# Kernel optimization log

Hardware: AMD Instinct MI355X
Metric: run time of the kernel (lower is better)

The kernel has to match this reference:

```python
import jax, jax.numpy as jnp
import numpy as np

DIM = 1024
HEADS = 16
HEAD_DIM = DIM // HEADS
D_FF = 4 * DIM
EPS = 1e-5


def layer_norm(x, gamma, beta):
    mu = jnp.mean(x, axis=-1, keepdims=True)
    var = jnp.var(x, axis=-1, keepdims=True)
    return (x - mu) * jax.lax.rsqrt(var + EPS) * gamma + beta


def linear_attention(x, w_qkv, b_qkv, w_out, b_out):
    B, S, D = x.shape
    qkv = x @ w_qkv + b_qkv  # [B,S,3D]
    qkv = qkv.reshape(B, S, 3, HEADS, HEAD_DIM)
    q, k, v = qkv[:, :, 0], qkv[:, :, 1], qkv[:, :, 2]  # [B,S,H,Dh]
    q = jax.nn.softmax(q, axis=-1)       # feature-dim softmax
    k = jax.nn.softmax(k, axis=1)        # sequence-dim softmax
    kv = jnp.einsum('bshd,bshe->bhde', k, v)   # [B,H,Dh,Dh]
    out = jnp.einsum('bshd,bhde->bshe', q, kv)  # [B,S,H,Dh]
    out = out.reshape(B, S, D)
    return out @ w_out + b_out


def setup_inputs() -> dict:
    key = jax.random.key(0)
    ks = jax.random.split(key, 10)
    s = lambda fan_in: 1.0 / np.sqrt(fan_in)
    return {
        'x': jax.random.normal(ks[0], (4, 4096, DIM), dtype=jnp.float32),
        'w_qkv': jax.random.normal(ks[1], (DIM, 3 * DIM), jnp.float32) * s(DIM),
        'b_qkv': jnp.zeros((3 * DIM,), jnp.float32),
        'w_attn_out': jax.random.normal(ks[2], (DIM, DIM), jnp.float32) * s(DIM),
        'b_attn_out': jnp.zeros((DIM,), jnp.float32),
        'w_ffn1': jax.random.normal(ks[3], (DIM, D_FF), jnp.float32) * s(DIM),
        'b_ffn1': jnp.zeros((D_FF,), jnp.float32),
        'w_ffn2': jax.random.normal(ks[4], (D_FF, DIM), jnp.float32) * s(D_FF),
        'b_ffn2': jnp.zeros((DIM,), jnp.float32),
        'g1': jnp.ones((DIM,), jnp.float32),
        'beta1': jnp.zeros((DIM,), jnp.float32),
        'g2': jnp.ones((DIM,), jnp.float32),
        'beta2': jnp.zeros((DIM,), jnp.float32),
    }


def reference(x, w_qkv, b_qkv, w_attn_out, b_attn_out, w_ffn1, b_ffn1,
              w_ffn2, b_ffn2, g1, beta1, g2, beta2):
    # h = attn(norm1(x)); out = x + ffn(norm2(x + h))  (dropout=0)
    h = linear_attention(layer_norm(x, g1, beta1), w_qkv, b_qkv, w_attn_out, b_attn_out)
    z = layer_norm(x + h, g2, beta2)
    delta = jax.nn.gelu(z @ w_ffn1 + b_ffn1, approximate=False) @ w_ffn2 + b_ffn2
    return x + delta
```

## Files before the change

kernel.cpp:

```cpp
#include <hip/hip_runtime.h>
#include <hip/hip_bf16.h>
#include <cstdint>
#include <cstddef>

#define DIMC 1024
#define HEADS 16
#define HD 64
#define DFF 4096
#define BB 4
#define SS 4096
#define NROWS (BB*SS)

typedef __bf16 bf16_t;
typedef __bf16 bf16x8 __attribute__((ext_vector_type(8)));
typedef __bf16 bf16x4 __attribute__((ext_vector_type(4)));
typedef float  f32x4  __attribute__((ext_vector_type(4)));

#define GLDS16(gp, lp) \
  __builtin_amdgcn_global_load_lds((const __attribute__((address_space(1))) void*)(gp), \
                                   (__attribute__((address_space(3))) void*)(lp), 16, 0, 0)

#define MFMA16(a, b, c) __builtin_amdgcn_mfma_f32_16x16x32_bf16((a), (b), (c), 0, 0, 0)

__device__ __forceinline__ float fast_erf(float x) {
  float ax = fabsf(x);
  float t  = __builtin_amdgcn_rcpf(fmaf(0.3275911f, ax, 1.0f));
  float p  = t * fmaf(t, fmaf(t, fmaf(t, fmaf(t, 1.061405429f, -1.453152027f),
                                      1.421413741f), -0.284496736f), 0.254829592f);
  float er = 1.0f - p * __expf(-ax * ax);
  return copysignf(er, x);
}

__global__ __launch_bounds__(256) void prep_kernel(const float* __restrict__ w_qkv,
                                                   const float* __restrict__ w_out,
                                                   const float* __restrict__ w_ffn1,
                                                   const float* __restrict__ w_ffn2,
                                                   bf16_t* __restrict__ WT_QKV,
                                                   bf16_t* __restrict__ WT_OUT,
                                                   bf16_t* __restrict__ WT_FFN1,
                                                   bf16_t* __restrict__ WT_FFN2,
                                                   const float* __restrict__ x,
                                                   const float* __restrict__ gamma,
                                                   const float* __restrict__ beta,
                                                   bf16_t* __restrict__ act1) {
  const int bid = blockIdx.x;
  if (bid < 12288) {
    const float* W; bf16_t* Wt; int K, N, bx, by;
    if (bid < 3072)      { W = w_qkv;  Wt = WT_QKV;  K = 1024; N = 3072; bx = bid % 96;           by = bid / 96; }
    else if (bid < 4096) { W = w_out;  Wt = WT_OUT;  K = 1024; N = 1024; bx = (bid - 3072) % 32;  by = (bid - 3072) / 32; }
    else if (bid < 8192) { W = w_ffn1; Wt = WT_FFN1; K = 1024; N = 4096; bx = (bid - 4096) % 128; by = (bid - 4096) / 128; }
    else                 { W = w_ffn2; Wt = WT_FFN2; K = 4096; N = 1024; bx = (bid - 8192) % 32;  by = (bid - 8192) / 32; }
    __shared__ float tile[32][33];
    const int tx = threadIdx.x & 31, ty = threadIdx.x >> 5;
    const int c0 = bx * 32, r0 = by * 32;
    #pragma unroll
    for (int i = 0; i < 32; i += 8)
      tile[ty + i][tx] = W[(long)(r0 + ty + i) * N + c0 + tx];
    __syncthreads();
    #pragma unroll
    for (int i = 0; i < 32; i += 8)
      Wt[(long)(c0 + ty + i) * K + r0 + tx] = (bf16_t)tile[tx][ty + i];
  } else {
    long r = bid - 12288;
    int t = threadIdx.x;
    float4 v = ((const float4*)(x + r * DIMC))[t];
    float s  = v.x + v.y + v.z + v.w;
    float sq = v.x * v.x + v.y * v.y + v.z * v.z + v.w * v.w;
    #pragma unroll
    for (int o = 32; o > 0; o >>= 1) { s += __shfl_xor(s, o); sq += __shfl_xor(sq, o); }
    __shared__ float red[8];
    if ((t & 63) == 0) { red[(t >> 6) * 2] = s; red[(t >> 6) * 2 + 1] = sq; }
    __syncthreads();
    s  = red[0] + red[2] + red[4] + red[6];
    sq = red[1] + red[3] + red[5] + red[7];
    float mu  = s * (1.0f / DIMC);
    float var = sq * (1.0f / DIMC) - mu * mu;
    float rs  = 1.0f / sqrtf(var + 1e-5f);
    float4 g  = ((const float4*)gamma)[t];
    float4 bb = ((const float4*)beta)[t];
    bf16x4 o;
    o[0] = (bf16_t)((v.x - mu) * rs * g.x + bb.x);
    o[1] = (bf16_t)((v.y - mu) * rs * g.y + bb.y);
    o[2] = (bf16_t)((v.z - mu) * rs * g.z + bb.z);
    o[3] = (bf16_t)((v.w - mu) * rs * g.w + bb.w);
    ((bf16x4*)(act1 + r * DIMC))[t] = o;
  }
}

__global__ __launch_bounds__(256) void ln_bf16(const bf16_t* __restrict__ in,
                                               const float* __restrict__ gamma,
                                               const float* __restrict__ beta,
                                               bf16_t* __restrict__ out) {
  long r = blockIdx.x;
  int t = threadIdx.x;
  bf16x4 v4 = ((const bf16x4*)(in + r * DIMC))[t];
  float v0 = v4[0], v1 = v4[1], v2 = v4[2], v3 = v4[3];
  float s  = v0 + v1 + v2 + v3;
  float sq = v0 * v0 + v1 * v1 + v2 * v2 + v3 * v3;
  #pragma unroll
  for (int o = 32; o > 0; o >>= 1) { s += __shfl_xor(s, o); sq += __shfl_xor(sq, o); }
  __shared__ float red[8];
  if ((t & 63) == 0) { red[(t >> 6) * 2] = s; red[(t >> 6) * 2 + 1] = sq; }
  __syncthreads();
  s  = red[0] + red[2] + red[4] + red[6];
  sq = red[1] + red[3] + red[5] + red[7];
  float mu  = s * (1.0f / DIMC);
  float var = sq * (1.0f / DIMC) - mu * mu;
  float rs  = 1.0f / sqrtf(var + 1e-5f);
  float4 g  = ((const float4*)gamma)[t];
  float4 bb = ((const float4*)beta)[t];
  bf16x4 o;
  o[0] = (bf16_t)((v0 - mu) * rs * g.x + bb.x);
  o[1] = (bf16_t)((v1 - mu) * rs * g.y + bb.y);
  o[2] = (bf16_t)((v2 - mu) * rs * g.z + bb.z);
  o[3] = (bf16_t)((v3 - mu) * rs * g.w + bb.w);
  ((bf16x4*)(out + r * DIMC))[t] = o;
}

template <int MODE>
__global__ __launch_bounds__(256, 2) void gemm_bt(const bf16_t* __restrict__ A,
                                                  const bf16_t* __restrict__ Bt,
                                                  const float* __restrict__ bias,
                                                  const float* __restrict__ resid,
                                                  void* __restrict__ outp,
                                                  int M, int N, int K, int lda, long bstride) {
  __shared__ bf16_t As[128 * 64];
  __shared__ bf16_t Bs[128 * 64];
  const int t = threadIdx.x;
  const int lane = t & 63;
  const int wave = t >> 6;

  const int nwg  = gridDim.x * gridDim.y;
  const int bid0 = blockIdx.y * gridDim.x + blockIdx.x;
  const int lg   = (bid0 & 7) * (nwg >> 3) + (bid0 >> 3);
  const int span = (int)gridDim.y << 2;
  const int gidx = lg / span;
  const int rem  = lg - gidx * span;
  const long arow0 = (long)(rem >> 2) * 128;
  const long brow0 = (long)((gidx << 2) + (rem & 3)) * 128;

  const bf16_t* BtB = Bt + (arow0 >> 12) * bstride;

  const int wm = (wave >> 1) * 64, wn = (wave & 1) * 64;

  f32x4 acc[4][4] = {};
  const int fr  = lane & 15;
  const int q4  = lane >> 4;
  const int frl = fr & 7;
  const int cr0 = ((q4    ) ^ frl) * 8;
  const int cr1 = ((q4 + 4) ^ frl) * 8;

  for (int kt = 0; kt < K; kt += 64) {
    #pragma unroll
    for (int p = 0; p < 4; ++p) {
      const int c = t + 256 * p;
      const int row = c >> 3;
      const int gch = ((c & 7) ^ (row & 7)) * 8;
      GLDS16(A   + (arow0 + row) * (long)lda + kt + gch, &As[c * 8]);
      GLDS16(BtB + (brow0 + row) * (long)K   + kt + gch, &Bs[c * 8]);
    }
    asm volatile("s_waitcnt vmcnt(0)" ::: "memory");
    __syncthreads();
    {
      bf16x8 a[4], b[4];
      #pragma unroll
      for (int i = 0; i < 4; ++i) {
        a[i] = *(const bf16x8*)&As[(wm + i * 16 + fr) * 64 + cr0];
        b[i] = *(const bf16x8*)&Bs[(wn + i * 16 + fr) * 64 + cr0];
      }
      #pragma unroll
      for (int i = 0; i < 4; ++i)
        #pragma unroll
        for (int j = 0; j < 4; ++j)
          acc[i][j] = MFMA16(a[i], b[j], acc[i][j]);
      #pragma unroll
      for (int i = 0; i < 4; ++i) {
        a[i] = *(const bf16x8*)&As[(wm + i * 16 + fr) * 64 + cr1];
        b[i] = *(const bf16x8*)&Bs[(wn + i * 16 + fr) * 64 + cr1];
      }
      #pragma unroll
      for (int i = 0; i < 4; ++i)
        #pragma unroll
        for (int j = 0; j < 4; ++j)
          acc[i][j] = MFMA16(a[i], b[j], acc[i][j]);
    }
    __syncthreads();
  }

  const int rq = q4 * 4;

  if (MODE == 3 && brow0 < 1024) {
    float bv[4];
    #pragma unroll
    for (int j = 0; j < 4; ++j) bv[j] = bias[brow0 + wn + j * 16 + fr];
    #pragma unroll
    for (int i = 0; i < 4; ++i) {
      #pragma unroll
      for (int r = 0; r < 4; ++r) {
        float v[4];
        #pragma unroll
        for (int j = 0; j < 4; ++j) v[j] = acc[i][j][r] + bv[j];
        float m = fmaxf(fmaxf(v[0], v[1]), fmaxf(v[2], v[3]));
        #pragma unroll
        for (int o = 1; o <= 8; o <<= 1) m = fmaxf(m, __shfl_xor(m, o));
        float e[4], s = 0.f;
        #pragma unroll
        for (int j = 0; j < 4; ++j) { e[j] = __expf(v[j] - m); s += e[j]; }
        #pragma unroll
        for (int o = 1; o <= 8; o <<= 1) s += __shfl_xor(s, o);
        float inv = 1.0f / s;
        long row = arow0 + wm + i * 16 + rq + r;
        #pragma unroll
        for (int j = 0; j < 4; ++j)
          ((bf16_t*)outp)[row * N + brow0 + wn + j * 16 + fr] = (bf16_t)(e[j] * inv);
      }
    }
  } else {
    #pragma unroll
    for (int i = 0; i < 4; ++i) {
      #pragma unroll
      for (int j = 0; j < 4; ++j) {
        long col = brow0 + wn + j * 16 + fr;
        float bv = bias[col];
        #pragma unroll
        for (int r = 0; r < 4; ++r) {
          long row = arow0 + wm + i * 16 + rq + r;
          float v = acc[i][j][r] + bv;
          if (MODE == 0 || MODE == 3) {
            ((bf16_t*)outp)[row * N + col] = (bf16_t)v;
          } else if (MODE == 1) {
            ((float*)outp)[row * N + col] = v + resid[row * N + col];
          } else if (MODE == 4) {
            ((bf16_t*)outp)[row * N + col] = (bf16_t)(v + resid[row * N + col]);
          } else {
            float g = 0.5f * v * (1.0f + fast_erf(v * 0.70710678118654752f));
            ((bf16_t*)outp)[row * N + col] = (bf16_t)g;
          }
        }
      }
    }
  }
}

__global__ __launch_bounds__(256) void kv_partial(const bf16_t* __restrict__ qkv,
                                                  float* __restrict__ kvp,
                                                  float* __restrict__ esump) {
  int bh = blockIdx.x, ch = blockIdx.y;
  int b = bh >> 4, h = bh & 15;
  int t = threadIdx.x;
  __shared__ float Kexp[64][65];
  __shared__ float Vs[64][66];
  int rowl = t >> 2, c0 = (t & 3) * 16;
  int dd = t >> 2, e0 = (t & 3) * 16;
  int lsq = (t & 3) * 16;
  float acc[16] = {};
  float esum = 0.f;
  for (int sb = 0; sb < 8; ++sb) {
    long s = (long)ch * 512 + sb * 64 + rowl;
    const bf16_t* base = qkv + ((long)b * SS + s) * 3072 + h * 64;
    bf16x8 k0 = *(const bf16x8*)(base + 1024 + c0);
    bf16x8 k1 = *(const bf16x8*)(base + 1024 + c0 + 8);
    bf16x8 v0 = *(const bf16x8*)(base + 2048 + c0);
    bf16x8 v1 = *(const bf16x8*)(base + 2048 + c0 + 8);
    __syncthreads();
    #pragma unroll
    for (int j = 0; j < 8; ++j) {
      Kexp[rowl][c0 + j]     = __expf((float)k0[j]);
      Kexp[rowl][c0 + 8 + j] = __expf((float)k1[j]);
      Vs[rowl][c0 + j]       = (float)v0[j];
      Vs[rowl][c0 + 8 + j]   = (float)v1[j];
    }
    __syncthreads();
    for (int ls = 0; ls < 64; ++ls) {
      float kd = Kexp[ls][dd];
      f32x4 va0 = *(const f32x4*)&Vs[ls][e0];
      f32x4 va1 = *(const f32x4*)&Vs[ls][e0 + 4];
      f32x4 va2 = *(const f32x4*)&Vs[ls][e0 + 8];
      f32x4 va3 = *(const f32x4*)&Vs[ls][e0 + 12];
      #pragma unroll
      for (int j = 0; j < 4; ++j) {
        acc[j]      += kd * va0[j];
        acc[j + 4]  += kd * va1[j];
        acc[j + 8]  += kd * va2[j];
        acc[j + 12] += kd * va3[j];
      }
    }
    #pragma unroll
    for (int l2 = 0; l2 < 16; ++l2) esum += Kexp[lsq + l2][dd];
  }
  float* dst = kvp + (long)(bh * 8 + ch) * 4096 + dd * 64 + e0;
  #pragma unroll
  for (int j = 0; j < 16; ++j) dst[j] = acc[j];
  esum += __shfl_xor(esum, 1);
  esum += __shfl_xor(esum, 2);
  if ((t & 3) == 0) esump[(long)(bh * 8 + ch) * 64 + dd] = esum;
}

__global__ void kv_reduce(const float* __restrict__ kvp, const float* __restrict__ esump,
                          bf16_t* __restrict__ kvN) {
  int bh = blockIdx.x, t = threadIdx.x;
  __shared__ float ei[64];
  if (t < 64) {
    float es = 0.f;
    #pragma unroll
    for (int c = 0; c < 8; ++c) es += esump[(long)(bh * 8 + c) * 64 + t];
    ei[t] = 1.0f / es;
  }
  __syncthreads();
  for (int p = t; p < 4096; p += 256) {
    int d = p >> 6;
    float s = 0.f;
    #pragma unroll
    for (int c = 0; c < 8; ++c) s += kvp[(long)(bh * 8 + c) * 4096 + p];
    kvN[(long)bh * 4096 + p] = (bf16_t)(s * ei[d]);
  }
}

__global__ __launch_bounds__(256) void kv_wout(const bf16_t* __restrict__ kvN,
                                               const bf16_t* __restrict__ WT_OUT,
                                               bf16_t* __restrict__ MBT) {
  const int jt = blockIdx.x;
  const int bh = blockIdx.y;
  const int b  = bh >> 4, h = bh & 15;
  const int t = threadIdx.x, lane = t & 63, wave = t >> 6;
  __shared__ bf16_t Ws[256 * 64];
  __shared__ bf16_t Ks[64 * 64];
  const int fr = lane & 15, q4 = lane >> 4, frl = fr & 7;
  const int cr0 = ((q4    ) ^ frl) * 8;
  const int cr1 = ((q4 + 4) ^ frl) * 8;
  #pragma unroll
  for (int p = 0; p < 8; ++p) {
    const int c = t + 256 * p;
    const int row = c >> 3;
    const int gch = ((c & 7) ^ (row & 7)) * 8;
    GLDS16(WT_OUT + (long)(jt * 256 + row) * 1024 + h * 64 + gch, &Ws[c * 8]);
  }
  #pragma unroll
  for (int p = 0; p < 2; ++p) {
    const int c = t + 256 * p;
    const int row = c >> 3;
    const int gch = ((c & 7) ^ (row & 7)) * 8;
    GLDS16(kvN + (long)bh * 4096 + row * 64 + gch, &Ks[c * 8]);
  }
  asm volatile("s_waitcnt vmcnt(0)" ::: "memory");
  __syncthreads();
  f32x4 acc[4][4] = {};
  const int wj = wave * 64;
  {
    bf16x8 a[4], bfr[4];
    #pragma unroll
    for (int i = 0; i < 4; ++i) {
      a[i]   = *(const bf16x8*)&Ws[(wj + i * 16 + fr) * 64 + cr0];
      bfr[i] = *(const bf16x8*)&Ks[(i * 16 + fr) * 64 + cr0];
    }
    #pragma unroll
    for (int i = 0; i < 4; ++i)
      #pragma unroll
      for (int j = 0; j < 4; ++j)
        acc[i][j] = MFMA16(a[i], bfr[j], acc[i][j]);
    #pragma unroll
    for (int i = 0; i < 4; ++i) {
      a[i]   = *(const bf16x8*)&Ws[(wj + i * 16 + fr) * 64 + cr1];
      bfr[i] = *(const bf16x8*)&Ks[(i * 16 + fr) * 64 + cr1];
    }
    #pragma unroll
    for (int i = 0; i < 4; ++i)
      #pragma unroll
      for (int j = 0; j < 4; ++j)
        acc[i][j] = MFMA16(a[i], bfr[j], acc[i][j]);
  }
  const int rq = q4 * 4;
  #pragma unroll
  for (int i = 0; i < 4; ++i)
    #pragma unroll
    for (int j = 0; j < 4; ++j)
      #pragma unroll
      for (int r = 0; r < 4; ++r)
        MBT[((long)b * 1024 + jt * 256 + wj + i * 16 + rq + r) * 1024 + h * 64 + j * 16 + fr]
            = (bf16_t)acc[i][j][r];
}

extern "C" void kernel_launch(void* const* d_in, const int* in_sizes, int n_in,
                              void* d_out, int out_size, void* d_ws, size_t ws_size,
                              hipStream_t stream) {
  (void)in_sizes; (void)n_in; (void)out_size;
  const float* x      = (const float*)d_in[0];
  const float* w_qkv  = (const float*)d_in[1];
  const float* b_qkv  = (const float*)d_in[2];
  const float* w_out  = (const float*)d_in[3];
  const float* b_out  = (const float*)d_in[4];
  const float* w_ffn1 = (const float*)d_in[5];
  const float* b_ffn1 = (const float*)d_in[6];
  const float* w_ffn2 = (const float*)d_in[7];
  const float* b_ffn2 = (const float*)d_in[8];
  const float* g1     = (const float*)d_in[9];
  const float* be1    = (const float*)d_in[10];
  const float* g2     = (const float*)d_in[11];
  const float* be2    = (const float*)d_in[12];

  char* ws = (char*)d_ws;
  constexpr size_t WT_QKV_OFF  = 0;
  constexpr size_t WT_OUT_OFF  = WT_QKV_OFF  + 6291456;
  constexpr size_t WT_FFN1_OFF = WT_OUT_OFF  + 2097152;
  constexpr size_t WT_FFN2_OFF = WT_FFN1_OFF + 8388608;
  constexpr size_t ESUMP_OFF   = WT_FFN2_OFF + 8388608;
  constexpr size_t KVP_OFF     = ESUMP_OFF   + 294912;
  constexpr size_t KVN_OFF     = KVP_OFF     + 8388608;
  constexpr size_t MBT_OFF     = KVN_OFF     + 524288;
  constexpr size_t ACT1_OFF    = MBT_OFF     + 8388608;
  constexpr size_t BIG_OFF     = ACT1_OFF    + 33554432;

  bf16_t* WT_QKV  = (bf16_t*)(ws + WT_QKV_OFF);
  bf16_t* WT_OUT  = (bf16_t*)(ws + WT_OUT_OFF);
  bf16_t* WT_FFN1 = (bf16_t*)(ws + WT_FFN1_OFF);
  bf16_t* WT_FFN2 = (bf16_t*)(ws + WT_FFN2_OFF);
  float*  ESUMP   = (float*) (ws + ESUMP_OFF);
  float*  KVP     = (float*) (ws + KVP_OFF);
  bf16_t* KVN     = (bf16_t*)(ws + KVN_OFF);
  bf16_t* MBT     = (bf16_t*)(ws + MBT_OFF);
  bf16_t* ACT1    = (bf16_t*)(ws + ACT1_OFF);
  bf16_t* QKV     = (bf16_t*)(ws + BIG_OFF);
  bf16_t* GACT    = (bf16_t*)(ws + BIG_OFF);
  bf16_t* YB      = (bf16_t*)d_out;

  const bool big_ws = ws_size >= (size_t)(BIG_OFF + 134217728ull);

  prep_kernel<<<12288 + NROWS, 256, 0, stream>>>(w_qkv, w_out, w_ffn1, w_ffn2,
                                                 WT_QKV, WT_OUT, WT_FFN1, WT_FFN2,
                                                 x, g1, be1, ACT1);

  gemm_bt<3><<<dim3(3072 / 128, NROWS / 128), 256, 0, stream>>>(ACT1, WT_QKV, b_qkv, nullptr, QKV,
                                                                NROWS, 3072, 1024, 1024, 0);

  kv_partial<<<dim3(64, 8), 256, 0, stream>>>(QKV, KVP, ESUMP);
  kv_reduce<<<64, 256, 0, stream>>>(KVP, ESUMP, KVN);
  kv_wout<<<dim3(4, 64), 256, 0, stream>>>(KVN, WT_OUT, MBT);

  gemm_bt<4><<<dim3(1024 / 128, NROWS / 128), 256, 0, stream>>>(QKV, MBT, b_out, x, YB,
                                                                NROWS, 1024, 1024, 3072, 1048576);

  ln_bf16<<<NROWS, 256, 0, stream>>>(YB, g2, be2, ACT1);

  if (big_ws) {
    gemm_bt<2><<<dim3(4096 / 128, NROWS / 128), 256, 0, stream>>>(ACT1, WT_FFN1, b_ffn1, nullptr, GACT,
                                                                  NROWS, 4096, 1024, 1024, 0);
    gemm_bt<1><<<dim3(1024 / 128, NROWS / 128), 256, 0, stream>>>(GACT, WT_FFN2, b_ffn2, x, (float*)d_out,
                                                                  NROWS, 1024, 4096, 4096, 0);
  } else {
    for (int c = 0; c < 2; ++c) {
      const long r0 = (long)c * 8192;
      gemm_bt<2><<<dim3(4096 / 128, 8192 / 128), 256, 0, stream>>>(
          ACT1 + r0 * 1024, WT_FFN1, b_ffn1, nullptr, GACT, 8192, 4096, 1024, 1024, 0);
      gemm_bt<1><<<dim3(1024 / 128, 8192 / 128), 256, 0, stream>>>(
          GACT, WT_FFN2, b_ffn2, x + r0 * 1024, (float*)d_out + r0 * 1024, 8192, 1024, 4096, 4096, 0);
    }
  }
}
```

Baseline: 606.6 us.

## Compute K^T V partials with bf16 MFMA instead of scalar FMAs

Rewrites kv_partial so each wave loads exp(K) and V fragments straight from global memory into registers and accumulates K^T V with 16x16x32 bf16 MFMA instructions. This drops the LDS staging and the two block barriers per step. Each wave computes a 64x16 output slice and recomputes exp(K) redundantly across the four waves. exp(K) is now rounded to bf16 before the product, which adds precision loss, and the global loads are strided 2-byte scalar gathers.

```diff
diff --git a/kernel.cpp b/kernel.cpp
--- a/kernel.cpp
+++ b/kernel.cpp
@@ -245,55 +245,55 @@
 __global__ __launch_bounds__(256) void kv_partial(const bf16_t* __restrict__ qkv,
                                                   float* __restrict__ kvp,
                                                   float* __restrict__ esump) {
-  int bh = blockIdx.x, ch = blockIdx.y;
-  int b = bh >> 4, h = bh & 15;
-  int t = threadIdx.x;
-  __shared__ float Kexp[64][65];
-  __shared__ float Vs[64][66];
-  int rowl = t >> 2, c0 = (t & 3) * 16;
-  int dd = t >> 2, e0 = (t & 3) * 16;
-  int lsq = (t & 3) * 16;
-  float acc[16] = {};
-  float esum = 0.f;
-  for (int sb = 0; sb < 8; ++sb) {
-    long s = (long)ch * 512 + sb * 64 + rowl;
-    const bf16_t* base = qkv + ((long)b * SS + s) * 3072 + h * 64;
-    bf16x8 k0 = *(const bf16x8*)(base + 1024 + c0);
-    bf16x8 k1 = *(const bf16x8*)(base + 1024 + c0 + 8);
-    bf16x8 v0 = *(const bf16x8*)(base + 2048 + c0);
-    bf16x8 v1 = *(const bf16x8*)(base + 2048 + c0 + 8);
-    __syncthreads();
-    #pragma unroll
-    for (int j = 0; j < 8; ++j) {
-      Kexp[rowl][c0 + j]     = __expf((float)k0[j]);
-      Kexp[rowl][c0 + 8 + j] = __expf((float)k1[j]);
-      Vs[rowl][c0 + j]       = (float)v0[j];
-      Vs[rowl][c0 + 8 + j]   = (float)v1[j];
-    }
-    __syncthreads();
-    for (int ls = 0; ls < 64; ++ls) {
-      float kd = Kexp[ls][dd];
-      f32x4 va0 = *(const f32x4*)&Vs[ls][e0];
-      f32x4 va1 = *(const f32x4*)&Vs[ls][e0 + 4];
-      f32x4 va2 = *(const f32x4*)&Vs[ls][e0 + 8];
-      f32x4 va3 = *(const f32x4*)&Vs[ls][e0 + 12];
-      #pragma unroll
-      for (int j = 0; j < 4; ++j) {
-        acc[j]      += kd * va0[j];
-        acc[j + 4]  += kd * va1[j];
-        acc[j + 8]  += kd * va2[j];
-        acc[j + 12] += kd * va3[j];
+  const int bh = blockIdx.x, ch = blockIdx.y;
+  const int b = bh >> 4, h = bh & 15;
+  const int t = threadIdx.x, lane = t & 63, w = t >> 6;
+  const int fr = lane & 15, q4 = lane >> 4;
+
+  const bf16_t* kbase = qkv + (long)b * SS * 3072 + 1024 + h * 64;
+  const bf16_t* vbase = qkv + (long)b * SS * 3072 + 2048 + h * 64;
+
+  f32x4 acc[4] = {};
+  float es[4] = {0.f, 0.f, 0.f, 0.f};
+
+  for (int sb = 0; sb < 16; ++sb) {
+    const long s0 = (long)ch * 512 + sb * 32 + q4 * 8;
+    bf16x8 af[4];
+    #pragma unroll
+    for (int i = 0; i < 4; ++i) {
+      const bf16_t* kp = kbase + s0 * 3072 + i * 16 + fr;
+      #pragma unroll
+      for (int j = 0; j < 8; ++j) {
+        float ex = __expf((float)kp[(long)j * 3072]);
+        af[i][j] = (bf16_t)ex;
+        es[i] += ex;
       }
     }
-    #pragma unroll
-    for (int l2 = 0; l2 < 16; ++l2) esum += Kexp[lsq + l2][dd];
-  }
-  float* dst = kvp + (long)(bh * 8 + ch) * 4096 + dd * 64 + e0;
-  #pragma unroll
-  for (int j = 0; j < 16; ++j) dst[j] = acc[j];
-  esum += __shfl_xor(esum, 1);
-  esum += __shfl_xor(esum, 2);
-  if ((t & 3) == 0) esump[(long)(bh * 8 + ch) * 64 + dd] = esum;
+    bf16x8 bfv;
+    const bf16_t* vp = vbase + s0 * 3072 + w * 16 + fr;
+    #pragma unroll
+    for (int j = 0; j < 8; ++j) bfv[j] = vp[(long)j * 3072];
+    #pragma unroll
+    for (int i = 0; i < 4; ++i) acc[i] = MFMA16(af[i], bfv, acc[i]);
+  }
+
+  float* dst = kvp + (long)(bh * 8 + ch) * 4096;
+  #pragma unroll
+  for (int i = 0; i < 4; ++i)
+    #pragma unroll
+    for (int r = 0; r < 4; ++r)
+      dst[(i * 16 + q4 * 4 + r) * 64 + w * 16 + fr] = acc[i][r];
+
+  #pragma unroll
+  for (int i = 0; i < 4; ++i) {
+    es[i] += __shfl_xor(es[i], 16);
+    es[i] += __shfl_xor(es[i], 32);
+  }
+  if (t < 16) {
+    #pragma unroll
+    for (int i = 0; i < 4; ++i)
+      esump[(long)(bh * 8 + ch) * 64 + i * 16 + t] = es[i];
+  }
 }
 
 __global__ void kv_reduce(const float* __restrict__ kvp, const float* __restrict__ esump,
```

Measured after the change: 546.3 us. -9.9%, faster.
